# Kernel tuning notes

Measured on AMD Instinct MI355X. Metric: run time of the kernel, lower is better.

The kernel has to match this reference:

```python
import jax, jax.numpy as jnp
import numpy as np

B, D, U = 256, 2048, 2048  # batch, input_dim, units
EPS = 1e-8


def setup_inputs() -> dict:
    key = jax.random.key(0)
    ks = jax.random.split(key, 20)
    sd = 1.0 / np.sqrt(D)
    su = 1.0 / np.sqrt(U)
    inp = {
        'x': jax.random.normal(ks[0], (B, D), jnp.float32),
        'h_prev': jax.random.normal(ks[1], (B, U), jnp.float32),
        'c_prev': jax.random.normal(ks[2], (B, U), jnp.float32),
        'n_prev': jax.random.uniform(ks[3], (B, U), jnp.float32),
        'm_prev': jax.random.normal(ks[4], (B, U), jnp.float32),
        # input-to-gate weights (Dense with bias), keras layout [in, out]
        'Wz': jax.random.normal(ks[5], (D, U), jnp.float32) * sd,
        'Wi': jax.random.normal(ks[6], (D, U), jnp.float32) * sd,
        'Wf': jax.random.normal(ks[7], (D, U), jnp.float32) * sd,
        'Wo': jax.random.normal(ks[8], (D, U), jnp.float32) * sd,
        'bz': jnp.zeros((U,), jnp.float32),
        'bi': jnp.zeros((U,), jnp.float32),
        'bf': jnp.zeros((U,), jnp.float32),
        'bo': jnp.zeros((U,), jnp.float32),
        # recurrent weights (Dense without bias)
        'Uz': jax.random.normal(ks[9], (U, U), jnp.float32) * su,
        'Ui': jax.random.normal(ks[10], (U, U), jnp.float32) * su,
        'Uf': jax.random.normal(ks[11], (U, U), jnp.float32) * su,
        'Uo': jax.random.normal(ks[12], (U, U), jnp.float32) * su,
    }
    return inp


def reference(x, h_prev, c_prev, n_prev, m_prev,
              Wz, Wi, Wf, Wo, bz, bi, bf, bo, Uz, Ui, Uf, Uo):
    # fuse the 8 small GEMMs into 2 wide GEMMs (same math, gates split after)
    W = jnp.concatenate([Wz, Wi, Wf, Wo], axis=1)      # [D, 4U]
    Uc = jnp.concatenate([Uz, Ui, Uf, Uo], axis=1)     # [U, 4U]
    b = jnp.concatenate([bz, bi, bf, bo], axis=0)      # [4U]
    pre = x @ W + h_prev @ Uc + b                      # [B, 4U]
    z_tilde, i_tilde, f_tilde, o_tilde = jnp.split(pre, 4, axis=1)

    # exponential-gate stabilization (forget_gate_type='exponential')
    m_t = jnp.maximum(i_tilde + m_prev, i_tilde)
    i_t = jnp.exp(i_tilde - m_t)
    f_t = jnp.exp(f_tilde + m_prev - m_t)

    o_t = jax.nn.sigmoid(o_tilde)
    z_t = jnp.tanh(z_tilde)

    c_t = f_t * c_prev + i_t * z_t
    n_t = f_t * n_prev + i_t
    h_t = o_t * (c_t / (n_t + EPS))
    return jnp.stack([h_t, c_t, n_t, m_t], axis=0)  # [4, B, U]
```

## Files before the change

### kernel.cpp

```cpp
#include <hip/hip_runtime.h>
#include <cstdint>
#include <cstddef>

#define B_   256
#define D_   2048
#define U_   2048
#define NTOT 8192
#define BN   64
#define BK   32
#define KC   1024

typedef _Float16 half8 __attribute__((ext_vector_type(8)));
typedef float floatx16 __attribute__((ext_vector_type(16)));

__global__ __launch_bounds__(256) void prep_kernel(
    const float* __restrict__ x, const float* __restrict__ h,
    _Float16* __restrict__ Ahi, _Float16* __restrict__ Alo)
{
    int gid   = blockIdx.x * 256 + threadIdx.x;
    int chunk = gid >> 8;
    int row   = gid & 255;
    int col0  = chunk * 8;
    const float* src = (col0 < D_) ? (x + row * D_ + col0)
                                   : (h + row * U_ + (col0 - D_));
    float4 v0 = *(const float4*)(src);
    float4 v1 = *(const float4*)(src + 4);
    float v[8] = {v0.x, v0.y, v0.z, v0.w, v1.x, v1.y, v1.z, v1.w};
    half8 hi, lo;
#pragma unroll
    for (int i = 0; i < 8; ++i) {
        _Float16 hv = (_Float16)v[i];
        hi[i] = hv;
        lo[i] = (_Float16)(v[i] - (float)hv);
    }
    int off = (chunk * 256 + row) * 8;
    *(half8*)(Ahi + off) = hi;
    *(half8*)(Alo + off) = lo;
}

__global__ __launch_bounds__(256) void gemm_kernel(
    const _Float16* __restrict__ Ahi, const _Float16* __restrict__ Alo,
    const float* __restrict__ Wz, const float* __restrict__ Wi,
    const float* __restrict__ Wf, const float* __restrict__ Wo,
    const float* __restrict__ Uz, const float* __restrict__ Ui,
    const float* __restrict__ Uf, const float* __restrict__ Uo,
    float* __restrict__ P)
{
    __shared__ __align__(16) _Float16 sAhi[4 * 256 * 8];
    __shared__ __align__(16) _Float16 sAlo[4 * 256 * 8];
    __shared__ __align__(16) _Float16 sBhi[64 * 40];
    __shared__ __align__(16) _Float16 sBlo[64 * 40];

    const int t    = threadIdx.x;
    const int w    = t >> 6;
    const int lane = t & 63;
    const int nblk = blockIdx.x;
    const int ks   = blockIdx.y;
    const int n0   = nblk * BN;
    const int g    = n0 >> 11;
    const int c0   = n0 & (U_ - 1);
    const int krow0  = (ks & 1) * KC;
    const int chunk0 = ks * (KC / 8);

    const float* wa = (g == 0) ? Wz : (g == 1) ? Wi : (g == 2) ? Wf : Wo;
    const float* ua = (g == 0) ? Uz : (g == 1) ? Ui : (g == 2) ? Uf : Uo;
    const float* Bm = (ks < 2) ? wa : ua;

    floatx16 acc[2][2] = {};

    const int lg = lane >> 5;
    const int lm = lane & 31;

    for (int kk = 0; kk < KC / BK; ++kk) {
        {
            int gch = chunk0 + kk * 4;
#pragma unroll
            for (int i = 0; i < 4; ++i) {
                int gidx = ((gch + i) * 256 + t) * 8;
                int lidx = (i * 256 + t) * 8;
                __builtin_amdgcn_global_load_lds(
                    (const __attribute__((address_space(1))) void*)(Ahi + gidx),
                    (__attribute__((address_space(3))) void*)(sAhi + lidx),
                    16, 0, 0);
                __builtin_amdgcn_global_load_lds(
                    (const __attribute__((address_space(1))) void*)(Alo + gidx),
                    (__attribute__((address_space(3))) void*)(sAlo + lidx),
                    16, 0, 0);
            }
        }
        {
            int n = lane;
            const float* bp = Bm + (size_t)(krow0 + kk * BK + w * 8) * U_ + (c0 + n);
            half8 bhi, blo;
#pragma unroll
            for (int j = 0; j < 8; ++j) {
                float v = bp[(size_t)j * U_];
                _Float16 hv = (_Float16)v;
                bhi[j] = hv;
                blo[j] = (_Float16)(v - (float)hv);
            }
            *(half8*)(&sBhi[n * 40 + w * 8]) = bhi;
            *(half8*)(&sBlo[n * 40 + w * 8]) = blo;
        }
        __syncthreads();
#pragma unroll
        for (int ksub = 0; ksub < 2; ++ksub) {
            half8 ah[2], al[2], bh[2], bl[2];
#pragma unroll
            for (int mt = 0; mt < 2; ++mt) {
                int row   = w * 64 + mt * 32 + lm;
                int chunk = ksub * 2 + lg;
                int off   = (chunk * 256 + row) * 8;
                ah[mt] = *(const half8*)(sAhi + off);
                al[mt] = *(const half8*)(sAlo + off);
            }
#pragma unroll
            for (int nt = 0; nt < 2; ++nt) {
                int n   = nt * 32 + lm;
                int off = n * 40 + ksub * 16 + lg * 8;
                bh[nt] = *(const half8*)(sBhi + off);
                bl[nt] = *(const half8*)(sBlo + off);
            }
#pragma unroll
            for (int mt = 0; mt < 2; ++mt)
#pragma unroll
                for (int nt = 0; nt < 2; ++nt) {
                    acc[mt][nt] = __builtin_amdgcn_mfma_f32_32x32x16_f16(
                        ah[mt], bh[nt], acc[mt][nt], 0, 0, 0);
                    acc[mt][nt] = __builtin_amdgcn_mfma_f32_32x32x16_f16(
                        ah[mt], bl[nt], acc[mt][nt], 0, 0, 0);
                    acc[mt][nt] = __builtin_amdgcn_mfma_f32_32x32x16_f16(
                        al[mt], bh[nt], acc[mt][nt], 0, 0, 0);
                }
        }
        __syncthreads();
    }

    float* Pks = P + (size_t)ks * ((size_t)B_ * NTOT);
#pragma unroll
    for (int mt = 0; mt < 2; ++mt)
#pragma unroll
        for (int nt = 0; nt < 2; ++nt) {
            int n = n0 + nt * 32 + lm;
#pragma unroll
            for (int r = 0; r < 16; ++r) {
                int m = w * 64 + mt * 32 + 4 * lg + (r & 3) + 8 * (r >> 2);
                Pks[(size_t)m * NTOT + n] = acc[mt][nt][r];
            }
        }
}

__global__ __launch_bounds__(256) void gates_kernel(
    const float* __restrict__ P,
    const float* __restrict__ c_prev, const float* __restrict__ n_prev,
    const float* __restrict__ m_prev,
    const float* __restrict__ bz, const float* __restrict__ bi,
    const float* __restrict__ bf, const float* __restrict__ bo,
    float* __restrict__ out)
{
    const size_t PS = (size_t)B_ * NTOT;
    const int OS = B_ * U_;
    int gid = blockIdx.x * 256 + threadIdx.x;
    int m = gid >> 9;
    int u = (gid & 511) * 4;

    float pre[4][4];
#pragma unroll
    for (int gi = 0; gi < 4; ++gi) {
        const float* base = P + (size_t)m * NTOT + gi * U_ + u;
        float4 s0 = *(const float4*)(base);
        float4 s1 = *(const float4*)(base + PS);
        float4 s2 = *(const float4*)(base + 2 * PS);
        float4 s3 = *(const float4*)(base + 3 * PS);
        pre[gi][0] = s0.x + s1.x + s2.x + s3.x;
        pre[gi][1] = s0.y + s1.y + s2.y + s3.y;
        pre[gi][2] = s0.z + s1.z + s2.z + s3.z;
        pre[gi][3] = s0.w + s1.w + s2.w + s3.w;
    }
    float4 bzv = *(const float4*)(bz + u);
    float4 biv = *(const float4*)(bi + u);
    float4 bfv = *(const float4*)(bf + u);
    float4 bov = *(const float4*)(bo + u);
    float bza[4] = {bzv.x, bzv.y, bzv.z, bzv.w};
    float bia[4] = {biv.x, biv.y, biv.z, biv.w};
    float bfa[4] = {bfv.x, bfv.y, bfv.z, bfv.w};
    float boa[4] = {bov.x, bov.y, bov.z, bov.w};

    float4 cp4 = *(const float4*)(c_prev + m * U_ + u);
    float4 np4 = *(const float4*)(n_prev + m * U_ + u);
    float4 mp4 = *(const float4*)(m_prev + m * U_ + u);
    float cpa[4] = {cp4.x, cp4.y, cp4.z, cp4.w};
    float npa[4] = {np4.x, np4.y, np4.z, np4.w};
    float mpa[4] = {mp4.x, mp4.y, mp4.z, mp4.w};

    float hr[4], cr[4], nr[4], mr[4];
#pragma unroll
    for (int e = 0; e < 4; ++e) {
        float zt = pre[0][e] + bza[e];
        float it = pre[1][e] + bia[e];
        float ft = pre[2][e] + bfa[e];
        float ot = pre[3][e] + boa[e];
        float mp = mpa[e];
        float m_t = fmaxf(it + mp, it);
        float i_t = expf(it - m_t);
        float f_t = expf(ft + mp - m_t);
        float o_t = 1.0f / (1.0f + expf(-ot));
        float z_t = tanhf(zt);
        float c_t = f_t * cpa[e] + i_t * z_t;
        float n_t = f_t * npa[e] + i_t;
        float h_t = o_t * (c_t / (n_t + 1e-8f));
        hr[e] = h_t; cr[e] = c_t; nr[e] = n_t; mr[e] = m_t;
    }
    float4 hv = {hr[0], hr[1], hr[2], hr[3]};
    float4 cv = {cr[0], cr[1], cr[2], cr[3]};
    float4 nv = {nr[0], nr[1], nr[2], nr[3]};
    float4 mv = {mr[0], mr[1], mr[2], mr[3]};
    *(float4*)(out + 0 * OS + m * U_ + u) = hv;
    *(float4*)(out + 1 * OS + m * U_ + u) = cv;
    *(float4*)(out + 2 * OS + m * U_ + u) = nv;
    *(float4*)(out + 3 * OS + m * U_ + u) = mv;
}

extern "C" void kernel_launch(void* const* d_in, const int* in_sizes, int n_in,
                              void* d_out, int out_size, void* d_ws, size_t ws_size,
                              hipStream_t stream)
{
    const float* x  = (const float*)d_in[0];
    const float* h  = (const float*)d_in[1];
    const float* cp = (const float*)d_in[2];
    const float* np = (const float*)d_in[3];
    const float* mp = (const float*)d_in[4];
    const float* Wz = (const float*)d_in[5];
    const float* Wi = (const float*)d_in[6];
    const float* Wf = (const float*)d_in[7];
    const float* Wo = (const float*)d_in[8];
    const float* bz = (const float*)d_in[9];
    const float* bi = (const float*)d_in[10];
    const float* bf = (const float*)d_in[11];
    const float* bo = (const float*)d_in[12];
    const float* Uz = (const float*)d_in[13];
    const float* Ui = (const float*)d_in[14];
    const float* Uf = (const float*)d_in[15];
    const float* Uo = (const float*)d_in[16];

    float* P = (float*)d_ws;
    _Float16* Ahi = (_Float16*)((char*)d_ws + (size_t)4 * B_ * NTOT * sizeof(float));
    _Float16* Alo = Ahi + (size_t)B_ * (D_ + U_);

    prep_kernel<<<512, 256, 0, stream>>>(x, h, Ahi, Alo);
    gemm_kernel<<<dim3(128, 4), 256, 0, stream>>>(Ahi, Alo,
        Wz, Wi, Wf, Wo, Uz, Ui, Uf, Uo, P);
    gates_kernel<<<512, 256, 0, stream>>>(P, cp, np, mp, bz, bi, bf, bo,
        (float*)d_out);
}
```

Before: 221.3 us.

## Drop fp16 split-precision terms, double-buffer GEMM tiles with async LDS loads

Removes the hi/lo fp16 error-compensation scheme, so the GEMM uses a single fp16 MFMA per tile instead of three and no longer builds a low-part activation buffer. Weights are now staged as fp32 into LDS via direct global-to-LDS loads in a double-buffered pipeline and converted to fp16 on read. Tiles change to BN=32/BK=64 with split-K reduced from 4 to 2, which halves the partial-sum traffic in the gates kernel. Dropping compensation lowers accuracy to plain fp16 inputs, which may exceed the reference tolerance.

```diff
diff --git a/kernel.cpp b/kernel.cpp
--- a/kernel.cpp
+++ b/kernel.cpp
@@ -6,16 +6,17 @@
 #define D_   2048
 #define U_   2048
 #define NTOT 8192
-#define BN   64
-#define BK   32
-#define KC   1024
+#define BN   32
+#define BK   64
+#define KC   2048
+#define ITERS (KC / BK)
 
 typedef _Float16 half8 __attribute__((ext_vector_type(8)));
 typedef float floatx16 __attribute__((ext_vector_type(16)));
 
 __global__ __launch_bounds__(256) void prep_kernel(
     const float* __restrict__ x, const float* __restrict__ h,
-    _Float16* __restrict__ Ahi, _Float16* __restrict__ Alo)
+    _Float16* __restrict__ Ahi)
 {
     int gid   = blockIdx.x * 256 + threadIdx.x;
     int chunk = gid >> 8;
@@ -26,127 +27,103 @@
     float4 v0 = *(const float4*)(src);
     float4 v1 = *(const float4*)(src + 4);
     float v[8] = {v0.x, v0.y, v0.z, v0.w, v1.x, v1.y, v1.z, v1.w};
-    half8 hi, lo;
-#pragma unroll
-    for (int i = 0; i < 8; ++i) {
-        _Float16 hv = (_Float16)v[i];
-        hi[i] = hv;
-        lo[i] = (_Float16)(v[i] - (float)hv);
-    }
-    int off = (chunk * 256 + row) * 8;
-    *(half8*)(Ahi + off) = hi;
-    *(half8*)(Alo + off) = lo;
+    half8 hi;
+#pragma unroll
+    for (int i = 0; i < 8; ++i) hi[i] = (_Float16)v[i];
+    *(half8*)(Ahi + (chunk * 256 + row) * 8) = hi;
 }
 
 __global__ __launch_bounds__(256) void gemm_kernel(
-    const _Float16* __restrict__ Ahi, const _Float16* __restrict__ Alo,
+    const _Float16* __restrict__ Ahi,
     const float* __restrict__ Wz, const float* __restrict__ Wi,
     const float* __restrict__ Wf, const float* __restrict__ Wo,
     const float* __restrict__ Uz, const float* __restrict__ Ui,
     const float* __restrict__ Uf, const float* __restrict__ Uo,
     float* __restrict__ P)
 {
-    __shared__ __align__(16) _Float16 sAhi[4 * 256 * 8];
-    __shared__ __align__(16) _Float16 sAlo[4 * 256 * 8];
-    __shared__ __align__(16) _Float16 sBhi[64 * 40];
-    __shared__ __align__(16) _Float16 sBlo[64 * 40];
+    __shared__ __align__(16) _Float16 sA[2][8 * 256 * 8];
+    __shared__ __align__(16) float    sB[2][BK * BN];
 
     const int t    = threadIdx.x;
     const int w    = t >> 6;
     const int lane = t & 63;
+    const int lg   = lane >> 5;
+    const int lm   = lane & 31;
+
     const int nblk = blockIdx.x;
     const int ks   = blockIdx.y;
     const int n0   = nblk * BN;
     const int g    = n0 >> 11;
     const int c0   = n0 & (U_ - 1);
-    const int krow0  = (ks & 1) * KC;
-    const int chunk0 = ks * (KC / 8);
-
-    const float* wa = (g == 0) ? Wz : (g == 1) ? Wi : (g == 2) ? Wf : Wo;
-    const float* ua = (g == 0) ? Uz : (g == 1) ? Ui : (g == 2) ? Uf : Uo;
-    const float* Bm = (ks < 2) ? wa : ua;
-
-    floatx16 acc[2][2] = {};
-
-    const int lg = lane >> 5;
-    const int lm = lane & 31;
-
-    for (int kk = 0; kk < KC / BK; ++kk) {
-        {
-            int gch = chunk0 + kk * 4;
-#pragma unroll
-            for (int i = 0; i < 4; ++i) {
-                int gidx = ((gch + i) * 256 + t) * 8;
-                int lidx = (i * 256 + t) * 8;
-                __builtin_amdgcn_global_load_lds(
-                    (const __attribute__((address_space(1))) void*)(Ahi + gidx),
-                    (__attribute__((address_space(3))) void*)(sAhi + lidx),
-                    16, 0, 0);
-                __builtin_amdgcn_global_load_lds(
-                    (const __attribute__((address_space(1))) void*)(Alo + gidx),
-                    (__attribute__((address_space(3))) void*)(sAlo + lidx),
-                    16, 0, 0);
+
+    const float* wsel[8] = {Wz, Wi, Wf, Wo, Uz, Ui, Uf, Uo};
+    const float* Bm = wsel[ks * 4 + g];
+    const int chunk0 = ks * 256;
+
+    const int arow_t = t;
+    const int bk_t   = t >> 3;
+    const int bc_t   = (t & 7) * 4;
+
+    floatx16 acc[2] = {};
+
+#define STAGE(kk, buf)                                                        \
+    {                                                                         \
+        int gch = chunk0 + (kk) * 8;                                          \
+        _Pragma("unroll")                                                     \
+        for (int i = 0; i < 8; ++i) {                                         \
+            int gidx = ((gch + i) * 256 + arow_t) * 8;                        \
+            int lidx = (i * 256 + arow_t) * 8;                                \
+            __builtin_amdgcn_global_load_lds(                                 \
+                (const __attribute__((address_space(1))) void*)(Ahi + gidx),  \
+                (__attribute__((address_space(3))) void*)(&sA[buf][lidx]),    \
+                16, 0, 0);                                                    \
+        }                                                                     \
+        _Pragma("unroll")                                                     \
+        for (int j = 0; j < 2; ++j) {                                         \
+            int krow = j * 32 + bk_t;                                         \
+            const float* src = Bm + (size_t)((kk) * BK + krow) * U_ + c0 + bc_t; \
+            __builtin_amdgcn_global_load_lds(                                 \
+                (const __attribute__((address_space(1))) void*)(src),         \
+                (__attribute__((address_space(3))) void*)(&sB[buf][krow * BN + bc_t]), \
+                16, 0, 0);                                                    \
+        }                                                                     \
+    }
+
+    STAGE(0, 0);
+    __syncthreads();
+
+    for (int kk = 0; kk < ITERS; ++kk) {
+        int cur = kk & 1;
+        if (kk + 1 < ITERS) STAGE(kk + 1, cur ^ 1);
+
+#pragma unroll
+        for (int kin = 0; kin < 4; ++kin) {
+            half8 a0, a1, bf;
+            {
+                int chunkIdx = kin * 2 + lg;
+                int row0 = w * 64 + lm;
+                a0 = *(const half8*)(&sA[cur][(chunkIdx * 256 + row0) * 8]);
+                a1 = *(const half8*)(&sA[cur][(chunkIdx * 256 + row0 + 32) * 8]);
             }
-        }
-        {
-            int n = lane;
-            const float* bp = Bm + (size_t)(krow0 + kk * BK + w * 8) * U_ + (c0 + n);
-            half8 bhi, blo;
 #pragma unroll
             for (int j = 0; j < 8; ++j) {
-                float v = bp[(size_t)j * U_];
-                _Float16 hv = (_Float16)v;
-                bhi[j] = hv;
-                blo[j] = (_Float16)(v - (float)hv);
+                float v = sB[cur][(kin * 16 + lg * 8 + j) * BN + lm];
+                bf[j] = (_Float16)v;
             }
-            *(half8*)(&sBhi[n * 40 + w * 8]) = bhi;
-            *(half8*)(&sBlo[n * 40 + w * 8]) = blo;
+            acc[0] = __builtin_amdgcn_mfma_f32_32x32x16_f16(a0, bf, acc[0], 0, 0, 0);
+            acc[1] = __builtin_amdgcn_mfma_f32_32x32x16_f16(a1, bf, acc[1], 0, 0, 0);
         }
         __syncthreads();
-#pragma unroll
-        for (int ksub = 0; ksub < 2; ++ksub) {
-            half8 ah[2], al[2], bh[2], bl[2];
-#pragma unroll
-            for (int mt = 0; mt < 2; ++mt) {
-                int row   = w * 64 + mt * 32 + lm;
-                int chunk = ksub * 2 + lg;
-                int off   = (chunk * 256 + row) * 8;
-                ah[mt] = *(const half8*)(sAhi + off);
-                al[mt] = *(const half8*)(sAlo + off);
-            }
-#pragma unroll
-            for (int nt = 0; nt < 2; ++nt) {
-                int n   = nt * 32 + lm;
-                int off = n * 40 + ksub * 16 + lg * 8;
-                bh[nt] = *(const half8*)(sBhi + off);
-                bl[nt] = *(const half8*)(sBlo + off);
-            }
-#pragma unroll
-            for (int mt = 0; mt < 2; ++mt)
-#pragma unroll
-                for (int nt = 0; nt < 2; ++nt) {
-                    acc[mt][nt] = __builtin_amdgcn_mfma_f32_32x32x16_f16(
-                        ah[mt], bh[nt], acc[mt][nt], 0, 0, 0);
-                    acc[mt][nt] = __builtin_amdgcn_mfma_f32_32x32x16_f16(
-                        ah[mt], bl[nt], acc[mt][nt], 0, 0, 0);
-                    acc[mt][nt] = __builtin_amdgcn_mfma_f32_32x32x16_f16(
-                        al[mt], bh[nt], acc[mt][nt], 0, 0, 0);
-                }
-        }
-        __syncthreads();
-    }
+    }
+#undef STAGE
 
     float* Pks = P + (size_t)ks * ((size_t)B_ * NTOT);
 #pragma unroll
     for (int mt = 0; mt < 2; ++mt)
 #pragma unroll
-        for (int nt = 0; nt < 2; ++nt) {
-            int n = n0 + nt * 32 + lm;
-#pragma unroll
-            for (int r = 0; r < 16; ++r) {
-                int m = w * 64 + mt * 32 + 4 * lg + (r & 3) + 8 * (r >> 2);
-                Pks[(size_t)m * NTOT + n] = acc[mt][nt][r];
-            }
+        for (int r = 0; r < 16; ++r) {
+            int m = w * 64 + mt * 32 + 4 * lg + (r & 3) + 8 * (r >> 2);
+            Pks[(size_t)m * NTOT + n0 + lm] = acc[mt][r];
         }
 }
 
@@ -170,12 +147,10 @@
         const float* base = P + (size_t)m * NTOT + gi * U_ + u;
         float4 s0 = *(const float4*)(base);
         float4 s1 = *(const float4*)(base + PS);
-        float4 s2 = *(const float4*)(base + 2 * PS);
-        float4 s3 = *(const float4*)(base + 3 * PS);
-        pre[gi][0] = s0.x + s1.x + s2.x + s3.x;
-        pre[gi][1] = s0.y + s1.y + s2.y + s3.y;
-        pre[gi][2] = s0.z + s1.z + s2.z + s3.z;
-        pre[gi][3] = s0.w + s1.w + s2.w + s3.w;
+        pre[gi][0] = s0.x + s1.x;
+        pre[gi][1] = s0.y + s1.y;
+        pre[gi][2] = s0.z + s1.z;
+        pre[gi][3] = s0.w + s1.w;
     }
     float4 bzv = *(const float4*)(bz + u);
     float4 biv = *(const float4*)(bi + u);
@@ -244,11 +219,10 @@
     const float* Uo = (const float*)d_in[16];
 
     float* P = (float*)d_ws;
-    _Float16* Ahi = (_Float16*)((char*)d_ws + (size_t)4 * B_ * NTOT * sizeof(float));
-    _Float16* Alo = Ahi + (size_t)B_ * (D_ + U_);
-
-    prep_kernel<<<512, 256, 0, stream>>>(x, h, Ahi, Alo);
-    gemm_kernel<<<dim3(128, 4), 256, 0, stream>>>(Ahi, Alo,
+    _Float16* Ahi = (_Float16*)((char*)d_ws + (size_t)2 * B_ * NTOT * sizeof(float));
+
+    prep_kernel<<<512, 256, 0, stream>>>(x, h, Ahi);
+    gemm_kernel<<<dim3(256, 2), 256, 0, stream>>>(Ahi,
         Wz, Wi, Wf, Wo, Uz, Ui, Uf, Uo, P);
     gates_kernel<<<512, 256, 0, stream>>>(P, cp, np, mp, bz, bi, bf, bo,
         (float*)d_out);
```

Measured after the change: 210.7 us. 1.05x faster.
